# Performance work log

Measured on AMD Instinct MI355X. Metric: run time of the kernel, lower is better.

The kernel has to match this reference:

```python
import jax, jax.numpy as jnp
import numpy as np

EMBED_DIM = 128
NUM_HEADS = 16
HEAD_DIM = EMBED_DIM // NUM_HEADS
SCALE = HEAD_DIM ** -0.5


def setup_inputs() -> dict:
    key = jax.random.key(0)
    ks = jax.random.split(key, 9)
    B, S, E = 4, 2048, EMBED_DIM
    s = 1.0 / np.sqrt(E)
    return {
        "x": jax.random.normal(ks[0], (B, S, E), dtype=jnp.float32),
        "Wq": jax.random.uniform(ks[1], (E, E), jnp.float32, -s, s),
        "bq": jax.random.uniform(ks[2], (E,), jnp.float32, -s, s),
        "Wk": jax.random.uniform(ks[3], (E, E), jnp.float32, -s, s),
        "bk": jax.random.uniform(ks[4], (E,), jnp.float32, -s, s),
        "Wv": jax.random.uniform(ks[5], (E, E), jnp.float32, -s, s),
        "bv": jax.random.uniform(ks[6], (E,), jnp.float32, -s, s),
        "Wo": jax.random.uniform(ks[7], (E, E), jnp.float32, -s, s),
        "bo": jax.random.uniform(ks[8], (E,), jnp.float32, -s, s),
    }


def reference(x, Wq, bq, Wk, bk, Wv, bv, Wo, bo):
    B, S, E = x.shape
    H, D = NUM_HEADS, HEAD_DIM
    # projections (torch Linear: x @ W.T + b)
    q = (x @ Wq.T + bq).reshape(B, S, H, D).transpose(0, 2, 1, 3)  # [B,H,S,D]
    k = (x @ Wk.T + bk).reshape(B, S, H, D).transpose(0, 2, 1, 3)
    v = (x @ Wv.T + bv).reshape(B, S, H, D).transpose(0, 2, 1, 3)
    scores = jnp.einsum("bhqd,bhkd->bhqk", q, k) * SCALE  # [B,H,S,S]
    causal_mask = jnp.triu(jnp.ones((S, S), dtype=bool), k=1)  # True above diag
    scores = jnp.where(causal_mask, jnp.float32(-1e9), scores)
    w = jax.nn.sigmoid(scores)
    w = w / jnp.sum(w, axis=-1, keepdims=True)  # sigmoid-sum normalization
    attn = jnp.einsum("bhqk,bhkd->bhqd", w, v)  # [B,H,S,D]
    attn = attn.transpose(0, 2, 1, 3).reshape(B, S, E)
    return attn @ Wo.T + bo
```

## Files before the change

kernel.cpp:

```cpp
#include <hip/hip_runtime.h>
#include <math.h>

#define EDIM 128
#define NHEAD 16
#define HDIM 8
#define SEQ 2048
#define BATCH 4
#define NROW (BATCH*SEQ)
#define QNEG (-0.35355339059327373f * 1.4426950408889634f)

#if __has_builtin(__builtin_amdgcn_exp2f)
#define EXP2F(x) __builtin_amdgcn_exp2f(x)
#else
#define EXP2F(x) exp2f(x)
#endif
#define RCPF(x) __builtin_amdgcn_rcpf(x)

typedef __attribute__((ext_vector_type(8))) short short8v;
typedef __attribute__((ext_vector_type(4))) short short4v;
typedef __attribute__((ext_vector_type(4))) float float4v;

union U16x8 { uint4 u; short8v s; };
union U16x4 { uint2 u; short4v s; };

#if __has_builtin(__builtin_amdgcn_mfma_f32_16x16x16bf16_1k)
#define MFMA_PV(a,b,c) __builtin_amdgcn_mfma_f32_16x16x16bf16_1k(a,b,c,0,0,0)
#else
static __device__ __forceinline__ float4v mfma_pv_asm(short4v a, short4v b, float4v c) {
  float4v d;
  asm("v_mfma_f32_16x16x16_bf16 %0, %1, %2, %3" : "=v"(d) : "v"(a), "v"(b), "v"(c));
  return d;
}
#define MFMA_PV(a,b,c) mfma_pv_asm(a,b,c)
#endif

__device__ __forceinline__ unsigned pk_bf16(float a, float b) {
  unsigned ua = __float_as_uint(a), ub = __float_as_uint(b);
  unsigned lo = (ua + 0x7fffu + ((ua >> 16) & 1u)) >> 16;
  unsigned hi = (ub + 0x7fffu + ((ub >> 16) & 1u)) & 0xffff0000u;
  return lo | hi;
}

__global__ __launch_bounds__(256)
void cast4_kernel(const float* __restrict__ W0, const float* __restrict__ W1,
                  const float* __restrict__ W2, const float* __restrict__ W3,
                  unsigned short* __restrict__ Wb)
{
  const float* W = (blockIdx.y == 0) ? W0 : (blockIdx.y == 1) ? W1
                 : (blockIdx.y == 2) ? W2 : W3;
  unsigned short* o = Wb + (size_t)blockIdx.y * (EDIM * EDIM);
  const int i = (blockIdx.x * 256 + threadIdx.x) * 4;
  const float4 f = *(const float4*)(W + i);
  uint2 p;
  p.x = pk_bf16(f.x, f.y);
  p.y = pk_bf16(f.z, f.w);
  *(uint2*)(o + i) = p;
}

__device__ __forceinline__
void stage16(const float* __restrict__ X, unsigned short* xs, int row0, int tid)
{
  const int r = tid >> 4, c16 = tid & 15;
  const float4* src = (const float4*)(X + (size_t)(row0 + r) * EDIM + c16 * 8);
  const float4 f0 = src[0], f1 = src[1];
  uint4 v;
  v.x = pk_bf16(f0.x, f0.y); v.y = pk_bf16(f0.z, f0.w);
  v.z = pk_bf16(f1.x, f1.y); v.w = pk_bf16(f1.z, f1.w);
  const unsigned addr = (unsigned)(r * 256 + c16 * 16) ^ (unsigned)((r & 7) << 4);
  *(uint4*)((char*)xs + addr) = v;
}

__device__ __forceinline__
void afrags(const unsigned short* xs, int lq, int qd, short8v a[4])
{
  #pragma unroll
  for (int kk = 0; kk < 4; ++kk) {
    const unsigned addr =
        (unsigned)(lq * 256 + kk * 64 + qd * 16) ^ (unsigned)((lq & 7) << 4);
    a[kk] = *(const short8v*)((const char*)xs + addr);
  }
}

template<int MODE>
__device__ __forceinline__
void proj_mfma(const float* __restrict__ X, const unsigned short* __restrict__ Wbm,
               const float* __restrict__ bias, void* __restrict__ out,
               int row0, int tid, unsigned short* xs, unsigned short* bnc)
{
  stage16(X, xs, row0, tid);
  __syncthreads();

  const int lane = tid & 63, wv = tid >> 6;
  const int lq = lane & 15, qd = lane >> 4;
  const int n0 = wv * 32;
  short8v a[4];
  afrags(xs, lq, qd, a);

  float4v D0 = {0.f, 0.f, 0.f, 0.f}, D1 = {0.f, 0.f, 0.f, 0.f};
  const unsigned short* wr0 = Wbm + (size_t)(n0 + lq) * EDIM + qd * 8;
  #pragma unroll
  for (int kk = 0; kk < 4; ++kk) {
    U16x8 b0, b1;
    b0.u = *(const uint4*)(wr0 + kk * 32);
    b1.u = *(const uint4*)(wr0 + 16 * EDIM + kk * 32);
    D0 = __builtin_amdgcn_mfma_f32_16x16x32_bf16(a[kk], b0.s, D0, 0, 0, 0);
    D1 = __builtin_amdgcn_mfma_f32_16x16x32_bf16(a[kk], b1.s, D1, 0, 0, 0);
  }

  const int nA = n0 + lq, nB = nA + 16;
  const float bzA = bias[nA], bzB = bias[nB];

  if (MODE == 3) {
    float* of = (float*)out + (size_t)(row0 + qd * 4) * EDIM + nA;
    #pragma unroll
    for (int r = 0; r < 4; ++r) {
      of[r * EDIM]      = D0[r] + bzA;
      of[r * EDIM + 16] = D1[r] + bzB;
    }
    return;
  }

  const int b_ = row0 >> 11, srel0 = row0 & (SEQ - 1);

  if (MODE == 2) {
    const int tg = srel0 >> 4;
    unsigned short* oU = (unsigned short*)out;
    {
      const int bh = b_ * NHEAD + (nA >> 3), dv = nA & 7;
      uint2 p;
      p.x = pk_bf16(D0[0] + bzA, D0[1] + bzA);
      p.y = pk_bf16(D0[2] + bzA, D0[3] + bzA);
      *(uint2*)(oU + (size_t)bh * (SEQ * HDIM) + tg * 128 + dv * 16 + qd * 4) = p;
    }
    {
      const int bh = b_ * NHEAD + (nB >> 3), dv = nB & 7;
      uint2 p;
      p.x = pk_bf16(D1[0] + bzB, D1[1] + bzB);
      p.y = pk_bf16(D1[2] + bzB, D1[3] + bzB);
      *(uint2*)(oU + (size_t)bh * (SEQ * HDIM) + tg * 128 + dv * 16 + qd * 4) = p;
    }
    return;
  }

  #pragma unroll
  for (int r = 0; r < 4; ++r) {
    float vA = D0[r] + bzA, vB = D1[r] + bzB;
    if (MODE == 0) { vA *= QNEG; vB *= QNEG; }
    const int m = qd * 4 + r;
    bnc[m * 20 + lq]       = (unsigned short)pk_bf16(vA, 0.f);
    bnc[320 + m * 20 + lq] = (unsigned short)pk_bf16(vB, 0.f);
  }
  __syncthreads();

  const int mm   = lane & 15;
  const int half = (lane >> 4) & 1;
  const int tile = lane >> 5;
  const unsigned short* sp = bnc + tile * 320 + mm * 20 + half * 8;
  const uint2 w0 = *(const uint2*)sp;
  const uint2 w1 = *(const uint2*)(sp + 4);
  const int bh = b_ * NHEAD + wv * 4 + tile * 2 + half;
  unsigned short* dp = (unsigned short*)out + ((size_t)bh * SEQ + srel0 + mm) * 8;
  *(uint4*)dp = make_uint4(w0.x, w0.y, w1.x, w1.y);
}

__global__ __launch_bounds__(256)
void qkv_kernel(const float* __restrict__ X, const unsigned short* __restrict__ Wb,
                const float* __restrict__ bq, const float* __restrict__ bk,
                const float* __restrict__ bv,
                unsigned* __restrict__ qb, unsigned* __restrict__ kb,
                unsigned* __restrict__ vb)
{
  __shared__ __align__(16) unsigned short xs[2048];
  __shared__ __align__(16) unsigned short bnc[4 * 640];
  const int tid = threadIdx.x;
  const int row0 = blockIdx.x * 16;
  unsigned short* myb = bnc + (tid >> 6) * 640;
  const int m = blockIdx.y;
  const unsigned short* wb = Wb + (size_t)m * EDIM * EDIM;
  if (m == 0)      proj_mfma<0>(X, wb, bq, (void*)qb, row0, tid, xs, myb);
  else if (m == 1) proj_mfma<1>(X, wb, bk, (void*)kb, row0, tid, xs, myb);
  else             proj_mfma<2>(X, wb, bv, (void*)vb, row0, tid, xs, myb);
}

__global__ __launch_bounds__(256)
void oproj_kernel(const float* __restrict__ A, const unsigned short* __restrict__ Wbo,
                  const float* __restrict__ bo, float* __restrict__ out)
{
  __shared__ __align__(16) unsigned short xs[2048];
  proj_mfma<3>(A, Wbo, bo, (void*)out, blockIdx.x * 16, threadIdx.x, xs, nullptr);
}

template<bool DIAG>
__device__ __forceinline__
float4v attn_step(short8v kf, short8v qf, short4v vf, float4v acc,
                  int laneq, int quad)
{
  const float4v z = {0.f, 0.f, 0.f, 0.f};
  float4v st = __builtin_amdgcn_mfma_f32_16x16x32_bf16(kf, qf, z, 0, 0, 0);
  unsigned rb[4];
  #pragma unroll
  for (int r = 0; r < 4; ++r) {
    float s = RCPF(1.f + EXP2F(st[r]));
    if (DIAG) s = (4 * quad + r <= laneq) ? s : 0.f;
    rb[r] = __float_as_uint(s) + 0x8000u;
  }
  U16x4 p;
  p.u.x = __builtin_amdgcn_perm(rb[1], rb[0], 0x07060302u);
  p.u.y = __builtin_amdgcn_perm(rb[3], rb[2], 0x07060302u);
  return MFMA_PV(p.s, vf, acc);
}

__device__ __forceinline__
short4v load_vfrag(const unsigned short* __restrict__ Vtbh, int t,
                   int quad, int d, bool is8)
{
  const unsigned short* p = Vtbh + t * 128 + d * 16 + 4 * quad;
  const uint2 v = *(const uint2*)p;
  U16x4 vf;
  vf.u.x = is8 ? 0x3F803F80u : v.x;
  vf.u.y = is8 ? 0x3F803F80u : v.y;
  return vf.s;
}

__device__ __forceinline__
void epilogue(float4v acc, int T, int bh, int laneq, int quad,
              float* __restrict__ out)
{
  const int b_ = bh >> 4, h = bh & 15;
  const int pidx = (quad * 16 + 8) << 2;
  #pragma unroll
  for (int r = 0; r < 4; ++r) {
    const float den = __int_as_float(
        __builtin_amdgcn_ds_bpermute(pidx, __float_as_int(acc[r])));
    const float val = acc[r] * RCPF(den);
    const int row = 16 * T + 4 * quad + r;
    if (laneq < 8)
      out[(size_t)(b_ * SEQ + row) * EDIM + h * HDIM + laneq] = val;
  }
}

__global__ __launch_bounds__(128, 8)
void attn_kernel(const unsigned* __restrict__ Qb, const unsigned* __restrict__ Kb,
                 const unsigned* __restrict__ Vb, float* __restrict__ out)
{
  __shared__ float cmb[2][64][4];

  const int bh    = blockIdx.x & 63;
  const int g     = blockIdx.x >> 6;
  const int w     = threadIdx.x >> 6;
  const int lane  = threadIdx.x & 63;
  const int laneq = lane & 15;
  const int quad  = lane >> 4;
  const int L = g, H = 127 - g;
  const int mL = (L + 1) >> 1, mH = (H + 1) >> 1;
  const int d   = laneq & 7;
  const bool is8 = (laneq == 8);

  const uint4* Kg = (const uint4*)Kb + (size_t)bh * 2048;
  const uint4* Qg = (const uint4*)Qb + (size_t)bh * 2048;
  const unsigned short* Vtbh = (const unsigned short*)Vb + (size_t)bh * SEQ * HDIM;

  U16x8 qfl, qfh;
  {
    const uint4 rl = Qg[16 * L + laneq];
    const uint4 rh = Qg[16 * H + laneq];
    qfl.u = (lane < 16) ? rl : make_uint4(0u, 0u, 0u, 0u);
    qfh.u = (lane < 16) ? rh : make_uint4(0u, 0u, 0u, 0u);
  }

  float4v accL = {0.f, 0.f, 0.f, 0.f};
  float4v accH = {0.f, 0.f, 0.f, 0.f};

  if (w == 0) {
    U16x8 kf; kf.u = Kg[laneq];
    short4v vf = load_vfrag(Vtbh, 0, quad, d, is8);
    #pragma unroll 2
    for (int t = 0; t < mH; ++t) {
      U16x8 kn; kn.u = Kg[16 * (t + 1) + laneq];
      short4v vn = load_vfrag(Vtbh, t + 1, quad, d, is8);
      if (t < mL) accL = attn_step<false>(kf.s, qfl.s, vf, accL, laneq, quad);
      accH = attn_step<false>(kf.s, qfh.s, vf, accH, laneq, quad);
      kf = kn; vf = vn;
    }
  } else {
    U16x8 kf; kf.u = Kg[16 * mL + laneq];
    short4v vf = load_vfrag(Vtbh, mL, quad, d, is8);
    #pragma unroll 2
    for (int t = mL; t < L; ++t) {
      U16x8 kn; kn.u = Kg[16 * (t + 1) + laneq];
      short4v vn = load_vfrag(Vtbh, t + 1, quad, d, is8);
      accL = attn_step<false>(kf.s, qfl.s, vf, accL, laneq, quad);
      kf = kn; vf = vn;
    }
    accL = attn_step<true>(kf.s, qfl.s, vf, accL, laneq, quad);
    kf.u = Kg[16 * mH + laneq];
    vf = load_vfrag(Vtbh, mH, quad, d, is8);
    #pragma unroll 2
    for (int t = mH; t < H; ++t) {
      U16x8 kn; kn.u = Kg[16 * (t + 1) + laneq];
      short4v vn = load_vfrag(Vtbh, t + 1, quad, d, is8);
      accH = attn_step<false>(kf.s, qfh.s, vf, accH, laneq, quad);
      kf = kn; vf = vn;
    }
    accH = attn_step<true>(kf.s, qfh.s, vf, accH, laneq, quad);

    *(float4*)&cmb[0][lane][0] = make_float4(accL[0], accL[1], accL[2], accL[3]);
    *(float4*)&cmb[1][lane][0] = make_float4(accH[0], accH[1], accH[2], accH[3]);
  }
  __syncthreads();

  if (w == 0) {
    const float4 pL = *(const float4*)&cmb[0][lane][0];
    const float4 pH = *(const float4*)&cmb[1][lane][0];
    accL[0] += pL.x; accL[1] += pL.y; accL[2] += pL.z; accL[3] += pL.w;
    accH[0] += pH.x; accH[1] += pH.y; accH[2] += pH.z; accH[3] += pH.w;
    epilogue(accL, L, bh, laneq, quad, out);
    epilogue(accH, H, bh, laneq, quad, out);
  }
}

extern "C" void kernel_launch(void* const* d_in, const int* in_sizes, int n_in,
                              void* d_out, int out_size, void* d_ws, size_t ws_size,
                              hipStream_t stream)
{
  const float* x  = (const float*)d_in[0];
  const float* Wq = (const float*)d_in[1];
  const float* bq = (const float*)d_in[2];
  const float* Wk = (const float*)d_in[3];
  const float* bk = (const float*)d_in[4];
  const float* Wv = (const float*)d_in[5];
  const float* bv = (const float*)d_in[6];
  const float* Wo = (const float*)d_in[7];
  const float* bo = (const float*)d_in[8];

  float* ws = (float*)d_ws;
  unsigned short* Wb = (unsigned short*)ws;
  float*    attn = ws + 65536;
  unsigned* Qb   = (unsigned*)(ws + 65536 + 1048576);
  unsigned* Kb   = Qb + (size_t)524288;
  unsigned* Vb   = Kb + (size_t)524288;

  cast4_kernel<<<dim3(16, 4), 256, 0, stream>>>(Wq, Wk, Wv, Wo, Wb);
  qkv_kernel<<<dim3(NROW / 16, 3), 256, 0, stream>>>(x, Wb, bq, bk, bv, Qb, Kb, Vb);
  attn_kernel<<<dim3(4096), 128, 0, stream>>>(Qb, Kb, Vb, attn);
  oproj_kernel<<<dim3(NROW / 16), 256, 0, stream>>>(attn, Wb + 3 * EDIM * EDIM, bo,
                                                    (float*)d_out);
}
```

Before: 123.1 us.

## Fuse weight bf16 cast into projection kernels and process 32 rows per block

Removes the separate weight-cast kernel launch. Each projection block now loads the fp32 weight matrix itself, converts it to bf16 into a swizzled LDS tile, and keeps the B fragments in registers. Each block also handles two 16-row tiles, which halves the grid and amortizes the weight conversion across 32 rows. The cost is redundant weight reads and conversion in every block, plus more LDS per block, which may reduce occupancy.

```diff
diff --git a/kernel.cpp b/kernel.cpp
--- a/kernel.cpp
+++ b/kernel.cpp
@@ -41,35 +41,6 @@
   return lo | hi;
 }
 
-__global__ __launch_bounds__(256)
-void cast4_kernel(const float* __restrict__ W0, const float* __restrict__ W1,
-                  const float* __restrict__ W2, const float* __restrict__ W3,
-                  unsigned short* __restrict__ Wb)
-{
-  const float* W = (blockIdx.y == 0) ? W0 : (blockIdx.y == 1) ? W1
-                 : (blockIdx.y == 2) ? W2 : W3;
-  unsigned short* o = Wb + (size_t)blockIdx.y * (EDIM * EDIM);
-  const int i = (blockIdx.x * 256 + threadIdx.x) * 4;
-  const float4 f = *(const float4*)(W + i);
-  uint2 p;
-  p.x = pk_bf16(f.x, f.y);
-  p.y = pk_bf16(f.z, f.w);
-  *(uint2*)(o + i) = p;
-}
-
-__device__ __forceinline__
-void stage16(const float* __restrict__ X, unsigned short* xs, int row0, int tid)
-{
-  const int r = tid >> 4, c16 = tid & 15;
-  const float4* src = (const float4*)(X + (size_t)(row0 + r) * EDIM + c16 * 8);
-  const float4 f0 = src[0], f1 = src[1];
-  uint4 v;
-  v.x = pk_bf16(f0.x, f0.y); v.y = pk_bf16(f0.z, f0.w);
-  v.z = pk_bf16(f1.x, f1.y); v.w = pk_bf16(f1.z, f1.w);
-  const unsigned addr = (unsigned)(r * 256 + c16 * 16) ^ (unsigned)((r & 7) << 4);
-  *(uint4*)((char*)xs + addr) = v;
-}
-
 __device__ __forceinline__
 void afrags(const unsigned short* xs, int lq, int qd, short8v a[4])
 {
@@ -83,111 +54,150 @@
 
 template<int MODE>
 __device__ __forceinline__
-void proj_mfma(const float* __restrict__ X, const unsigned short* __restrict__ Wbm,
-               const float* __restrict__ bias, void* __restrict__ out,
-               int row0, int tid, unsigned short* xs, unsigned short* bnc)
-{
-  stage16(X, xs, row0, tid);
+void proj32(const float* __restrict__ X, const float* __restrict__ W,
+            const float* __restrict__ bias, void* __restrict__ out,
+            int row0, int tid,
+            unsigned short* wlds, unsigned short* xs, unsigned short* bnc)
+{
+  {
+    const int n = tid >> 1, h = (tid & 1) * 64;
+    const float4* src = (const float4*)(W + (size_t)n * EDIM + h);
+    const unsigned xr = (unsigned)((n & 7) << 4);
+    #pragma unroll
+    for (int j = 0; j < 8; ++j) {
+      const float4 f0 = src[2 * j], f1 = src[2 * j + 1];
+      const uint4 v = make_uint4(pk_bf16(f0.x, f0.y), pk_bf16(f0.z, f0.w),
+                                 pk_bf16(f1.x, f1.y), pk_bf16(f1.z, f1.w));
+      *(uint4*)((char*)wlds + ((unsigned)(n * 256 + h * 2 + j * 16) ^ xr)) = v;
+    }
+  }
+  {
+    const int r = tid >> 3, c = tid & 7;
+    const float4* src = (const float4*)(X + (size_t)(row0 + r) * EDIM + c * 16);
+    const unsigned xr = (unsigned)((r & 7) << 4);
+    const float4 f0 = src[0], f1 = src[1], f2 = src[2], f3 = src[3];
+    const uint4 v0 = make_uint4(pk_bf16(f0.x, f0.y), pk_bf16(f0.z, f0.w),
+                                pk_bf16(f1.x, f1.y), pk_bf16(f1.z, f1.w));
+    const uint4 v1 = make_uint4(pk_bf16(f2.x, f2.y), pk_bf16(f2.z, f2.w),
+                                pk_bf16(f3.x, f3.y), pk_bf16(f3.z, f3.w));
+    *(uint4*)((char*)xs + ((unsigned)(r * 256 + c * 32) ^ xr)) = v0;
+    *(uint4*)((char*)xs + ((unsigned)(r * 256 + c * 32 + 16) ^ xr)) = v1;
+  }
   __syncthreads();
 
   const int lane = tid & 63, wv = tid >> 6;
   const int lq = lane & 15, qd = lane >> 4;
   const int n0 = wv * 32;
-  short8v a[4];
-  afrags(xs, lq, qd, a);
-
-  float4v D0 = {0.f, 0.f, 0.f, 0.f}, D1 = {0.f, 0.f, 0.f, 0.f};
-  const unsigned short* wr0 = Wbm + (size_t)(n0 + lq) * EDIM + qd * 8;
+
+  short8v b0[4], b1[4];
   #pragma unroll
   for (int kk = 0; kk < 4; ++kk) {
-    U16x8 b0, b1;
-    b0.u = *(const uint4*)(wr0 + kk * 32);
-    b1.u = *(const uint4*)(wr0 + 16 * EDIM + kk * 32);
-    D0 = __builtin_amdgcn_mfma_f32_16x16x32_bf16(a[kk], b0.s, D0, 0, 0, 0);
-    D1 = __builtin_amdgcn_mfma_f32_16x16x32_bf16(a[kk], b1.s, D1, 0, 0, 0);
+    const unsigned ad = (unsigned)((n0 + lq) * 256 + kk * 64 + qd * 16)
+                      ^ (unsigned)((lq & 7) << 4);
+    b0[kk] = *(const short8v*)((const char*)wlds + ad);
+    b1[kk] = *(const short8v*)((const char*)wlds + ad + 4096);
   }
 
   const int nA = n0 + lq, nB = nA + 16;
   const float bzA = bias[nA], bzB = bias[nB];
-
-  if (MODE == 3) {
-    float* of = (float*)out + (size_t)(row0 + qd * 4) * EDIM + nA;
+  const int b_ = row0 >> 11;
+
+  #pragma unroll
+  for (int rt = 0; rt < 2; ++rt) {
+    const int rowt = row0 + rt * 16;
+    short8v a[4];
+    afrags(xs + rt * 2048, lq, qd, a);
+
+    float4v D0 = {0.f, 0.f, 0.f, 0.f}, D1 = {0.f, 0.f, 0.f, 0.f};
+    #pragma unroll
+    for (int kk = 0; kk < 4; ++kk) {
+      D0 = __builtin_amdgcn_mfma_f32_16x16x32_bf16(a[kk], b0[kk], D0, 0, 0, 0);
+      D1 = __builtin_amdgcn_mfma_f32_16x16x32_bf16(a[kk], b1[kk], D1, 0, 0, 0);
+    }
+
+    if (MODE == 3) {
+      float* of = (float*)out + (size_t)(rowt + qd * 4) * EDIM + nA;
+      #pragma unroll
+      for (int r = 0; r < 4; ++r) {
+        of[r * EDIM]      = D0[r] + bzA;
+        of[r * EDIM + 16] = D1[r] + bzB;
+      }
+      continue;
+    }
+
+    const int srel = rowt & (SEQ - 1);
+
+    if (MODE == 2) {
+      const int tg = srel >> 4;
+      unsigned short* oU = (unsigned short*)out;
+      {
+        const int bh = b_ * NHEAD + (nA >> 3), dv = nA & 7;
+        uint2 p;
+        p.x = pk_bf16(D0[0] + bzA, D0[1] + bzA);
+        p.y = pk_bf16(D0[2] + bzA, D0[3] + bzA);
+        *(uint2*)(oU + (size_t)bh * (SEQ * HDIM) + tg * 128 + dv * 16 + qd * 4) = p;
+      }
+      {
+        const int bh = b_ * NHEAD + (nB >> 3), dv = nB & 7;
+        uint2 p;
+        p.x = pk_bf16(D1[0] + bzB, D1[1] + bzB);
+        p.y = pk_bf16(D1[2] + bzB, D1[3] + bzB);
+        *(uint2*)(oU + (size_t)bh * (SEQ * HDIM) + tg * 128 + dv * 16 + qd * 4) = p;
+      }
+      continue;
+    }
+
     #pragma unroll
     for (int r = 0; r < 4; ++r) {
-      of[r * EDIM]      = D0[r] + bzA;
-      of[r * EDIM + 16] = D1[r] + bzB;
-    }
-    return;
-  }
-
-  const int b_ = row0 >> 11, srel0 = row0 & (SEQ - 1);
-
-  if (MODE == 2) {
-    const int tg = srel0 >> 4;
-    unsigned short* oU = (unsigned short*)out;
-    {
-      const int bh = b_ * NHEAD + (nA >> 3), dv = nA & 7;
-      uint2 p;
-      p.x = pk_bf16(D0[0] + bzA, D0[1] + bzA);
-      p.y = pk_bf16(D0[2] + bzA, D0[3] + bzA);
-      *(uint2*)(oU + (size_t)bh * (SEQ * HDIM) + tg * 128 + dv * 16 + qd * 4) = p;
-    }
-    {
-      const int bh = b_ * NHEAD + (nB >> 3), dv = nB & 7;
-      uint2 p;
-      p.x = pk_bf16(D1[0] + bzB, D1[1] + bzB);
-      p.y = pk_bf16(D1[2] + bzB, D1[3] + bzB);
-      *(uint2*)(oU + (size_t)bh * (SEQ * HDIM) + tg * 128 + dv * 16 + qd * 4) = p;
-    }
-    return;
-  }
-
-  #pragma unroll
-  for (int r = 0; r < 4; ++r) {
-    float vA = D0[r] + bzA, vB = D1[r] + bzB;
-    if (MODE == 0) { vA *= QNEG; vB *= QNEG; }
-    const int m = qd * 4 + r;
-    bnc[m * 20 + lq]       = (unsigned short)pk_bf16(vA, 0.f);
-    bnc[320 + m * 20 + lq] = (unsigned short)pk_bf16(vB, 0.f);
-  }
-  __syncthreads();
-
-  const int mm   = lane & 15;
-  const int half = (lane >> 4) & 1;
-  const int tile = lane >> 5;
-  const unsigned short* sp = bnc + tile * 320 + mm * 20 + half * 8;
-  const uint2 w0 = *(const uint2*)sp;
-  const uint2 w1 = *(const uint2*)(sp + 4);
-  const int bh = b_ * NHEAD + wv * 4 + tile * 2 + half;
-  unsigned short* dp = (unsigned short*)out + ((size_t)bh * SEQ + srel0 + mm) * 8;
-  *(uint4*)dp = make_uint4(w0.x, w0.y, w1.x, w1.y);
+      float vA = D0[r] + bzA, vB = D1[r] + bzB;
+      if (MODE == 0) { vA *= QNEG; vB *= QNEG; }
+      const int m = qd * 4 + r;
+      bnc[m * 20 + lq]       = (unsigned short)pk_bf16(vA, 0.f);
+      bnc[320 + m * 20 + lq] = (unsigned short)pk_bf16(vB, 0.f);
+    }
+    __syncthreads();
+
+    const int mm   = lane & 15;
+    const int half = (lane >> 4) & 1;
+    const int tile = lane >> 5;
+    const unsigned short* sp = bnc + tile * 320 + mm * 20 + half * 8;
+    const uint2 w0 = *(const uint2*)sp;
+    const uint2 w1 = *(const uint2*)(sp + 4);
+    const int bh = b_ * NHEAD + wv * 4 + tile * 2 + half;
+    unsigned short* dp = (unsigned short*)out + ((size_t)bh * SEQ + srel + mm) * 8;
+    *(uint4*)dp = make_uint4(w0.x, w0.y, w1.x, w1.y);
+    __syncthreads();
+  }
 }
 
 __global__ __launch_bounds__(256)
-void qkv_kernel(const float* __restrict__ X, const unsigned short* __restrict__ Wb,
+void qkv_kernel(const float* __restrict__ X,
+                const float* __restrict__ Wq, const float* __restrict__ Wk,
+                const float* __restrict__ Wv,
                 const float* __restrict__ bq, const float* __restrict__ bk,
                 const float* __restrict__ bv,
                 unsigned* __restrict__ qb, unsigned* __restrict__ kb,
                 unsigned* __restrict__ vb)
 {
-  __shared__ __align__(16) unsigned short xs[2048];
+  __shared__ __align__(16) unsigned short wlds[16384];
+  __shared__ __align__(16) unsigned short xs[4096];
   __shared__ __align__(16) unsigned short bnc[4 * 640];
   const int tid = threadIdx.x;
-  const int row0 = blockIdx.x * 16;
+  const int row0 = blockIdx.x * 32;
   unsigned short* myb = bnc + (tid >> 6) * 640;
   const int m = blockIdx.y;
-  const unsigned short* wb = Wb + (size_t)m * EDIM * EDIM;
-  if (m == 0)      proj_mfma<0>(X, wb, bq, (void*)qb, row0, tid, xs, myb);
-  else if (m == 1) proj_mfma<1>(X, wb, bk, (void*)kb, row0, tid, xs, myb);
-  else             proj_mfma<2>(X, wb, bv, (void*)vb, row0, tid, xs, myb);
+  if (m == 0)      proj32<0>(X, Wq, bq, (void*)qb, row0, tid, wlds, xs, myb);
+  else if (m == 1) proj32<1>(X, Wk, bk, (void*)kb, row0, tid, wlds, xs, myb);
+  else             proj32<2>(X, Wv, bv, (void*)vb, row0, tid, wlds, xs, myb);
 }
 
 __global__ __launch_bounds__(256)
-void oproj_kernel(const float* __restrict__ A, const unsigned short* __restrict__ Wbo,
+void oproj_kernel(const float* __restrict__ A, const float* __restrict__ Wo,
                   const float* __restrict__ bo, float* __restrict__ out)
 {
-  __shared__ __align__(16) unsigned short xs[2048];
-  proj_mfma<3>(A, Wbo, bo, (void*)out, blockIdx.x * 16, threadIdx.x, xs, nullptr);
+  __shared__ __align__(16) unsigned short wlds[16384];
+  __shared__ __align__(16) unsigned short xs[4096];
+  proj32<3>(A, Wo, bo, (void*)out, blockIdx.x * 32, threadIdx.x, wlds, xs, nullptr);
 }
 
 template<bool DIAG>
@@ -334,15 +344,13 @@
   const float* bo = (const float*)d_in[8];
 
   float* ws = (float*)d_ws;
-  unsigned short* Wb = (unsigned short*)ws;
   float*    attn = ws + 65536;
   unsigned* Qb   = (unsigned*)(ws + 65536 + 1048576);
   unsigned* Kb   = Qb + (size_t)524288;
   unsigned* Vb   = Kb + (size_t)524288;
 
-  cast4_kernel<<<dim3(16, 4), 256, 0, stream>>>(Wq, Wk, Wv, Wo, Wb);
-  qkv_kernel<<<dim3(NROW / 16, 3), 256, 0, stream>>>(x, Wb, bq, bk, bv, Qb, Kb, Vb);
+  qkv_kernel<<<dim3(NROW / 32, 3), 256, 0, stream>>>(x, Wq, Wk, Wv, bq, bk, bv,
+                                                     Qb, Kb, Vb);
   attn_kernel<<<dim3(4096), 128, 0, stream>>>(Qb, Kb, Vb, attn);
-  oproj_kernel<<<dim3(NROW / 16), 256, 0, stream>>>(attn, Wb + 3 * EDIM * EDIM, bo,
-                                                    (float*)d_out);
-}
+  oproj_kernel<<<dim3(NROW / 32), 256, 0, stream>>>(attn, Wo, bo, (float*)d_out);
+}
```

Result: no change. 121.8 us (-1.0%).
